# Optimization experiments

Hardware: AMD Instinct MI355X
Metric: run time of the kernel (lower is better)

The kernel has to match this reference:

```python
import jax, jax.numpy as jnp
import numpy as np
import math

S, B, H, NH, HD = 2048, 1, 4096, 32, 128
ROT = HD // 2  # 2D RoPE: each half of head_dim gets its own rotary embedding


def _rotate_half(x):
    x1, x2 = jnp.split(x, 2, axis=-1)
    return jnp.concatenate((-x2, x1), axis=-1)


def _rope_tables(max_pos, dim):
    inv_freq = 1.0 / (10000.0 ** (jnp.arange(0, dim, 2, dtype=jnp.float32) / dim))
    freqs = jnp.arange(max_pos, dtype=jnp.float32)[:, None] * inv_freq[None, :]  # [P, dim/2]
    emb = jnp.concatenate((freqs, freqs), axis=-1)  # [P, dim]
    return jnp.cos(emb), jnp.sin(emb)


def _apply_rope(q, k, cos_t, sin_t, pid):
    # q,k: [S,B,NH,ROT]; pid: [S,B]
    c = cos_t[pid][:, :, None, :]  # [S,B,1,ROT]
    s = sin_t[pid][:, :, None, :]
    return q * c + _rotate_half(q) * s, k * c + _rotate_half(k) * s


def setup_inputs() -> dict:
    key = jax.random.key(0)
    k1, k2, k3, k4, k5 = jax.random.split(key, 5)
    hidden_states = jax.random.normal(k1, (S, B, H), dtype=jnp.float32)
    pos = jnp.arange(S, dtype=jnp.int32)[None, :]          # [1,S] standard positions
    blk = jnp.zeros((1, S), dtype=jnp.int32)                # block positions (pre-gmask all zeros)
    position_ids = jnp.stack([pos, blk], axis=1)            # [B,2,S]
    # causal mask: True = masked out
    attention_mask = jnp.triu(jnp.ones((S, S), dtype=bool), k=1)[None, None]  # [B,1,S,S]
    Wqkv = jax.random.normal(k2, (3 * H, H), dtype=jnp.float32) * 0.02
    bqkv = jax.random.normal(k3, (3 * H,), dtype=jnp.float32) * 0.02
    Wd = jax.random.normal(k4, (H, H), dtype=jnp.float32) * 0.02
    bd = jax.random.normal(k5, (H,), dtype=jnp.float32) * 0.02
    return {"hidden_states": hidden_states, "position_ids": position_ids,
            "attention_mask": attention_mask, "layer_id": 5,
            "Wqkv": Wqkv, "bqkv": bqkv, "Wd": Wd, "bd": bd}


def reference(hidden_states, position_ids, attention_mask, layer_id, Wqkv, bqkv, Wd, bd):
    # QKV projection: [S,B,H] -> [S,B,NH,3*HD]
    mixed = hidden_states @ Wqkv.T + bqkv
    mixed = mixed.reshape(S, B, NH, 3 * HD)
    q, k, v = jnp.split(mixed, 3, axis=-1)  # each [S,B,NH,HD]

    # 2D rotary position embedding on the two head-dim halves
    q1, q2 = jnp.split(q, 2, axis=-1)
    k1, k2 = jnp.split(k, 2, axis=-1)
    cos_t, sin_t = _rope_tables(S, ROT)
    pid = position_ids[:, 0, :].T   # [S,B]
    bid = position_ids[:, 1, :].T   # [S,B]
    q1, k1 = _apply_rope(q1, k1, cos_t, sin_t, pid)
    q2, k2 = _apply_rope(q2, k2, cos_t, sin_t, bid)
    q = jnp.concatenate([q1, q2], axis=-1)
    k = jnp.concatenate([k1, k2], axis=-1)

    # layer-scaled attention scores
    coeff = float(layer_id + 1)
    q = q / (math.sqrt(HD) * coeff)
    scores = jnp.einsum('sbnd,tbnd->bnst', q, k)  # [B,NH,S,S]
    scores = jnp.where(attention_mask, jnp.float32(-10000.0), scores)
    scores = scores.astype(jnp.float32) * coeff
    probs = jax.nn.softmax(scores, axis=-1).astype(hidden_states.dtype)

    ctx = jnp.einsum('bnst,tbnd->sbnd', probs, v).reshape(S, B, NH * HD)
    return ctx @ Wd.T + bd  # [S,B,H]
```

## Files before the change

### kernel.cpp

```cpp
#include <hip/hip_runtime.h>


#define S_LEN 2048
#define NHEAD 32
#define HDIM 128
#define HID 4096

typedef float f32x4 __attribute__((ext_vector_type(4)));
typedef __bf16 bf16x8 __attribute__((ext_vector_type(8)));
typedef __bf16 bf16x4 __attribute__((ext_vector_type(4)));
typedef _Float16 f16x4 __attribute__((ext_vector_type(4)));
typedef _Float16 f16x8 __attribute__((ext_vector_type(8)));

__device__ __forceinline__ void gload16(const void* g, void* l) {
  __builtin_amdgcn_global_load_lds(
      (const __attribute__((address_space(1))) void*)g,
      (__attribute__((address_space(3))) void*)l, 16, 0, 0);
}

__global__ __launch_bounds__(256) void cvt_f32_bf16_kernel(
    const float* __restrict__ in, __bf16* __restrict__ out, int n4) {
  int i = blockIdx.x * 256 + threadIdx.x;
  if (i >= n4) return;
  f32x4 v = *(const f32x4*)(in + (size_t)i * 4);
  bf16x4 o;
  o[0] = (__bf16)v[0]; o[1] = (__bf16)v[1];
  o[2] = (__bf16)v[2]; o[3] = (__bf16)v[3];
  *(bf16x4*)(out + (size_t)i * 4) = o;
}

__device__ __forceinline__ void stage_half(const __bf16* __restrict__ G,
                                           int grow0, int Kstride, int kofs,
                                           __bf16* lds_half, int tid) {
#pragma unroll
  for (int i = 0; i < 2; ++i) {
    int idx = i * 512 + tid;
    int rr = idx >> 3;
    int offp = (idx & 7) * 16;
    int off = offp ^ ((rr & 7) << 4);
    const char* src =
        (const char*)(G + (size_t)(grow0 + rr) * Kstride + kofs) + off;
    char* dst = (char*)lds_half + idx * 16;
    gload16(src, dst);
  }
}

__device__ __forceinline__ bf16x8 ldsfrag(const __bf16* hb, int rowin, int ks,
                                          int lg) {
  int off = ((ks * 64 + lg * 16) ^ ((rowin & 7) << 4));
  return *(const bf16x8*)((const char*)hb + rowin * 128 + off);
}

#define READ_A(DST, SLOT)                                                     \
  _Pragma("unroll") for (int mi = 0; mi < 4; ++mi)                            \
      _Pragma("unroll") for (int ks = 0; ks < 2; ++ks) DST[mi][ks] =          \
      ldsfrag(SLOT, wm * 64 + mi * 16 + lr, ks, lg);

#define READ_B(DST, SLOT)                                                     \
  _Pragma("unroll") for (int nj = 0; nj < 2; ++nj)                            \
      _Pragma("unroll") for (int ks = 0; ks < 2; ++ks) DST[nj][ks] =          \
      ldsfrag(SLOT, wn * 32 + nj * 16 + lr, ks, lg);

#define MFMA_Q(MH, NH, AFR, BFR)                                              \
  __builtin_amdgcn_s_setprio(1);                                              \
  _Pragma("unroll") for (int mi = 0; mi < 4; ++mi)                            \
      _Pragma("unroll") for (int nj = 0; nj < 2; ++nj)                        \
          _Pragma("unroll") for (int ks = 0; ks < 2; ++ks)                    \
              acc[MH][NH][mi][nj] =                                           \
      __builtin_amdgcn_mfma_f32_16x16x32_bf16(AFR[mi][ks], BFR[nj][ks],       \
                                              acc[MH][NH][mi][nj], 0, 0, 0);  \
  __builtin_amdgcn_s_setprio(0);

#define BAR asm volatile("s_barrier" ::: "memory");
#define LGKM0                                                                 \
  asm volatile("s_waitcnt lgkmcnt(0)" ::: "memory");                          \
  __builtin_amdgcn_sched_barrier(0);

template <int OUT_MODE>
__global__ __launch_bounds__(512, 2) void gemm256_kernel(
    const __bf16* __restrict__ A, const __bf16* __restrict__ B,
    const float* __restrict__ bias, void* __restrict__ Cout, int M, int N,
    int Kstride, int klen, int mtiles, int ksplit) {
  __shared__ __align__(16) __bf16 As[2][2][128 * 64];
  __shared__ __align__(16) __bf16 Bs[2][2][128 * 64];
  const int tid = threadIdx.x;
  int bid = blockIdx.x;
  int kh = 0;
  if (ksplit == 2) { kh = bid & 1; bid >>= 1; }
  const int kbase = kh * klen;
  int per_patch = mtiles * 8;
  int p = bid / per_patch, r = bid % per_patch;
  int mt = r % mtiles, nt = p * 8 + r / mtiles;
  int m0 = mt * 256, n0 = nt * 256;
  const int wid = tid >> 6, l = tid & 63;
  const int wm = wid >> 2, wn = wid & 3;
  const int lr = l & 15, lg = l >> 4;
  const int nk = klen >> 6;

  f32x4 acc[2][2][4][2];
#pragma unroll
  for (int a = 0; a < 2; ++a)
#pragma unroll
    for (int b = 0; b < 2; ++b)
#pragma unroll
      for (int c = 0; c < 4; ++c)
#pragma unroll
        for (int d = 0; d < 2; ++d) acc[a][b][c][d] = 0.f;

  stage_half(A, m0, Kstride, kbase, &As[0][0][0], tid);
  stage_half(B, n0, Kstride, kbase, &Bs[0][0][0], tid);
  stage_half(B, n0 + 128, Kstride, kbase, &Bs[0][1][0], tid);
  stage_half(A, m0 + 128, Kstride, kbase, &As[0][1][0], tid);
  if (nk > 1) {
    stage_half(A, m0, Kstride, kbase + 64, &As[1][0][0], tid);
    stage_half(B, n0, Kstride, kbase + 64, &Bs[1][0][0], tid);
    stage_half(B, n0 + 128, Kstride, kbase + 64, &Bs[1][1][0], tid);
    asm volatile("s_waitcnt vmcnt(6)" ::: "memory");
  } else {
    asm volatile("s_waitcnt vmcnt(0)" ::: "memory");
  }
  BAR;

  for (int t = 0; t < nk; ++t) {
    const int cur = t & 1, nxt = cur ^ 1;
    const int kt1 = kbase + (t + 1) * 64;
    const int kt2 = kbase + (t + 2) * 64;
    const bool s1 = (t + 1 < nk), s2 = (t + 2 < nk);
    bf16x8 a[4][2], b0[2][2], b1[2][2];

    READ_A(a, &As[cur][0][0]);
    READ_B(b0, &Bs[cur][0][0]);
    if (s1) stage_half(A, m0 + 128, Kstride, kt1, &As[nxt][1][0], tid);
    BAR;
    LGKM0;
    MFMA_Q(0, 0, a, b0);
    BAR;

    READ_B(b1, &Bs[cur][1][0]);
    if (s2) stage_half(A, m0, Kstride, kt2, &As[cur][0][0], tid);
    BAR;
    LGKM0;
    MFMA_Q(0, 1, a, b1);
    BAR;

    READ_A(a, &As[cur][1][0]);
    if (s2) stage_half(B, n0 + 128, Kstride, kt2, &Bs[cur][1][0], tid);
    BAR;
    LGKM0;
    MFMA_Q(1, 1, a, b1);
    BAR;

    if (s2) stage_half(B, n0, Kstride, kt2, &Bs[cur][0][0], tid);
    BAR;
    MFMA_Q(1, 0, a, b0);
    if (s2)
      asm volatile("s_waitcnt vmcnt(6)" ::: "memory");
    else
      asm volatile("s_waitcnt vmcnt(0)" ::: "memory");
    BAR;
  }

  float* outF = (float*)Cout;
  if (OUT_MODE == 2) outF += (size_t)kh * M * N;
#pragma unroll
  for (int mh = 0; mh < 2; ++mh)
#pragma unroll
    for (int nh = 0; nh < 2; ++nh)
#pragma unroll
      for (int mi = 0; mi < 4; ++mi)
#pragma unroll
        for (int nj = 0; nj < 2; ++nj) {
          int row = m0 + mh * 128 + wm * 64 + mi * 16 + lg * 4;
          int col = n0 + nh * 128 + wn * 32 + nj * 16 + lr;
          float bv = (OUT_MODE == 2) ? 0.f : bias[col];
          f32x4 v = acc[mh][nh][mi][nj];
#pragma unroll
          for (int j = 0; j < 4; ++j) {
            float o = v[j] + bv;
            if (OUT_MODE == 1)
              ((__bf16*)Cout)[(size_t)(row + j) * N + col] = (__bf16)o;
            else
              outF[(size_t)(row + j) * N + col] = o;
          }
        }
}

__global__ __launch_bounds__(256) void reduce_addbias_kernel(
    const float* __restrict__ p0, const float* __restrict__ p1,
    const float* __restrict__ bias, float* __restrict__ out) {
  int i = blockIdx.x * 256 + threadIdx.x;
  int col = (i * 4) & (HID - 1);
  f32x4 a = *(const f32x4*)(p0 + (size_t)i * 4);
  f32x4 b = *(const f32x4*)(p1 + (size_t)i * 4);
  f32x4 c = *(const f32x4*)(bias + col);
  a = a + b + c;
  *(f32x4*)(out + (size_t)i * 4) = a;
}

__global__ __launch_bounds__(256) void rope_kernel(
    const __bf16* __restrict__ qkv, const int* __restrict__ pos_ids,
    __bf16* __restrict__ Q, __bf16* __restrict__ K, _Float16* __restrict__ VT) {
  int h = blockIdx.x & 31, sb = blockIdx.x >> 5;
  int s0 = sb * 64;
  int t = threadIdx.x;
  __shared__ float cs[64][2][2][32];
  __shared__ _Float16 vs[64][132];

  for (int idx = t; idx < 64 * 64; idx += 256) {
    int sl = idx >> 6, half = (idx >> 5) & 1, i = idx & 31;
    int p = pos_ids[half * S_LEN + s0 + sl];
    float f = powf(10000.f, -(float)i / 32.f);
    float ang = (float)p * f;
    cs[sl][half][0][i] = cosf(ang);
    cs[sl][half][1][i] = sinf(ang);
  }
#pragma unroll
  for (int c = 0; c < 4; c++) {
    int chunk = c * 256 + t;
    int slv = chunk >> 4, co = (chunk & 15) * 8;
    const __bf16* vsrc =
        qkv + (size_t)(s0 + slv) * (NHEAD * 3 * HDIM) + h * 384 + 256 + co;
    bf16x8 vv = *(const bf16x8*)vsrc;
    f16x4 a, b;
#pragma unroll
    for (int j = 0; j < 4; j++) {
      a[j] = (_Float16)(float)vv[j];
      b[j] = (_Float16)(float)vv[4 + j];
    }
    *(f16x4*)&vs[slv][co] = a;
    *(f16x4*)&vs[slv][co + 4] = b;
  }
  __syncthreads();

  {
    int sl = t >> 2, role = t & 3;
    int isK = role >> 1, half = role & 1;
    const __bf16* src = qkv + (size_t)(s0 + sl) * (NHEAD * 3 * HDIM) + h * 384 +
                        isK * 128 + half * 64;
    float scale = isK ? 1.f : 0.08838834764831845f;
    float x[64];
    bf16x8 buf[8];
#pragma unroll
    for (int c = 0; c < 8; c++) buf[c] = *(const bf16x8*)(src + c * 8);
#pragma unroll
    for (int c = 0; c < 8; c++)
#pragma unroll
      for (int j = 0; j < 8; j++) x[c * 8 + j] = (float)buf[c][j];
    bf16x8 ob[8];
#pragma unroll
    for (int i = 0; i < 64; i++) {
      int ii = i & 31;
      float cv = cs[sl][half][0][ii], sv = cs[sl][half][1][ii];
      float partner = (i < 32) ? x[i + 32] : x[i - 32];
      float sgn = (i < 32) ? -1.f : 1.f;
      float o = (x[i] * cv + sgn * partner * sv) * scale;
      ob[i >> 3][i & 7] = (__bf16)o;
    }
    __bf16* dst = (isK ? K : Q) + ((size_t)h * S_LEN + s0 + sl) * HDIM + half * 64;
#pragma unroll
    for (int c = 0; c < 8; c++) *(bf16x8*)(dst + c * 8) = ob[c];
  }

#pragma unroll
  for (int c = 0; c < 4; c++) {
    int chunk = c * 256 + t;
    int d = chunk >> 3, so = (chunk & 7) * 8;
    f16x8 o;
#pragma unroll
    for (int j = 0; j < 8; j++) o[j] = vs[so + j][d];
    *(f16x8*)(VT + ((size_t)h * HDIM + d) * S_LEN + s0 + so) = o;
  }
}

__global__ __launch_bounds__(256, 2) void attn_kernel(
    const __bf16* __restrict__ Q, const __bf16* __restrict__ K,
    const _Float16* __restrict__ VT, __bf16* __restrict__ ctx) {
  int b = blockIdx.x;
  int h = b & 31;
  int qb = 15 - (b >> 5);
  int w = threadIdx.x >> 6, l = threadIdx.x & 63;
  int lr = l & 15, lg = l >> 4;
  int q0 = qb * 128 + w * 32;
  const __bf16* Qh = Q + (size_t)h * S_LEN * HDIM;
  const __bf16* Kh = K + (size_t)h * S_LEN * HDIM;
  const _Float16* Vh = VT + (size_t)h * HDIM * S_LEN;

  bf16x8 qfA[4], qfB[4];
#pragma unroll
  for (int kk = 0; kk < 4; kk++) {
    qfA[kk] = *(const bf16x8*)(Qh + (size_t)(q0 + lr) * HDIM + kk * 32 + lg * 8);
    qfB[kk] =
        *(const bf16x8*)(Qh + (size_t)(q0 + 16 + lr) * HDIM + kk * 32 + lg * 8);
  }

  f32x4 accA[8], accB[8];
#pragma unroll
  for (int tt = 0; tt < 8; tt++) { accA[tt] = 0.f; accB[tt] = 0.f; }
  float mA = -INFINITY, lsA = 0.f, mB = -INFINITY, lsB = 0.f;
  int qgA = q0 + lr, qgB = q0 + 16 + lr;
  int qmax = q0 + 31;

  for (int kv0 = 0; kv0 <= qmax; kv0 += 16) {
    f32x4 stA = 0.f, stB = 0.f;
#pragma unroll
    for (int kk = 0; kk < 4; kk++) {
      bf16x8 kf =
          *(const bf16x8*)(Kh + (size_t)(kv0 + lr) * HDIM + kk * 32 + lg * 8);
      stA = __builtin_amdgcn_mfma_f32_16x16x32_bf16(kf, qfA[kk], stA, 0, 0, 0);
      stB = __builtin_amdgcn_mfma_f32_16x16x32_bf16(kf, qfB[kk], stB, 0, 0, 0);
    }
    float tmA = -INFINITY, tmB = -INFINITY;
#pragma unroll
    for (int j = 0; j < 4; j++) {
      int kvg = kv0 + lg * 4 + j;
      if (kvg > qgA) stA[j] = -INFINITY;
      if (kvg > qgB) stB[j] = -INFINITY;
      tmA = fmaxf(tmA, stA[j]);
      tmB = fmaxf(tmB, stB[j]);
    }
    tmA = fmaxf(tmA, __shfl_xor(tmA, 16));
    tmA = fmaxf(tmA, __shfl_xor(tmA, 32));
    tmB = fmaxf(tmB, __shfl_xor(tmB, 16));
    tmB = fmaxf(tmB, __shfl_xor(tmB, 32));
    int need = __any((tmA > mA) || (tmB > mB));
    float mnA = fmaxf(mA, tmA), mnB = fmaxf(mB, tmB);

    f16x4 paA, paB;
    float tsA = 0.f, tsB = 0.f;
#pragma unroll
    for (int j = 0; j < 4; j++) {
      float pA = __expf(stA[j] - mnA);
      float pB = __expf(stB[j] - mnB);
      tsA += pA; tsB += pB;
      paA[j] = (_Float16)pA; paB[j] = (_Float16)pB;
    }
    tsA += __shfl_xor(tsA, 16);
    tsA += __shfl_xor(tsA, 32);
    tsB += __shfl_xor(tsB, 16);
    tsB += __shfl_xor(tsB, 32);

    if (need) {
      float scA = __expf(mA - mnA), scB = __expf(mB - mnB);
      lsA = lsA * scA + tsA;
      lsB = lsB * scB + tsB;
      float sAj[4], sBj[4];
#pragma unroll
      for (int j = 0; j < 4; j++) {
        sAj[j] = __shfl(scA, lg * 4 + j);
        sBj[j] = __shfl(scB, lg * 4 + j);
      }
#pragma unroll
      for (int tt = 0; tt < 8; tt++)
#pragma unroll
        for (int j = 0; j < 4; j++) {
          accA[tt][j] *= sAj[j];
          accB[tt][j] *= sBj[j];
        }
    } else {
      lsA += tsA;
      lsB += tsB;
    }
    mA = mnA; mB = mnB;

#pragma unroll
    for (int tt = 0; tt < 8; tt++) {
      f16x4 vb =
          *(const f16x4*)(Vh + (size_t)(tt * 16 + lr) * S_LEN + kv0 + lg * 4);
      accA[tt] = __builtin_amdgcn_mfma_f32_16x16x16f16(paA, vb, accA[tt], 0, 0, 0);
      accB[tt] = __builtin_amdgcn_mfma_f32_16x16x16f16(paB, vb, accB[tt], 0, 0, 0);
    }
  }

  float rA[4], rB[4];
#pragma unroll
  for (int j = 0; j < 4; j++) {
    rA[j] = 1.f / __shfl(lsA, lg * 4 + j);
    rB[j] = 1.f / __shfl(lsB, lg * 4 + j);
  }
#pragma unroll
  for (int tt = 0; tt < 8; tt++) {
#pragma unroll
    for (int j = 0; j < 4; j++) {
      int qoA = q0 + lg * 4 + j;
      int qoB = q0 + 16 + lg * 4 + j;
      ctx[(size_t)qoA * (NHEAD * HDIM) + h * HDIM + tt * 16 + lr] =
          (__bf16)(accA[tt][j] * rA[j]);
      ctx[(size_t)qoB * (NHEAD * HDIM) + h * HDIM + tt * 16 + lr] =
          (__bf16)(accB[tt][j] * rB[j]);
    }
  }
}

extern "C" void kernel_launch(void* const* d_in, const int* in_sizes, int n_in,
                              void* d_out, int out_size, void* d_ws,
                              size_t ws_size, hipStream_t stream) {
  const float* hs = (const float*)d_in[0];
  const int* pos_ids = (const int*)d_in[1];
  const float* Wqkv = (const float*)d_in[4];
  const float* bqkv = (const float*)d_in[5];
  const float* Wd = (const float*)d_in[6];
  const float* bd = (const float*)d_in[7];
  float* out = (float*)d_out;

  char* ws = (char*)d_ws;
  constexpr size_t OFF_W = 16777216ULL;
  constexpr size_t OFF_QKV = OFF_W + 100663296ULL;
  constexpr size_t OFF_Q = OFF_QKV + 50331648ULL;
  constexpr size_t OFF_K = OFF_Q + 16777216ULL;
  constexpr size_t OFF_V = OFF_K + 16777216ULL;
  __bf16* hsb = (__bf16*)(ws);
  __bf16* wqkvb = (__bf16*)(ws + OFF_W);
  __bf16* wdb = (__bf16*)(ws + OFF_W);
  float* pk = (float*)(ws + OFF_W + 33554432ULL);
  __bf16* qkvb = (__bf16*)(ws + OFF_QKV);
  __bf16* ctxb = qkvb;
  __bf16* Qb = (__bf16*)(ws + OFF_Q);
  __bf16* Kb = (__bf16*)(ws + OFF_K);
  _Float16* Vtb = (_Float16*)(ws + OFF_V);

  cvt_f32_bf16_kernel<<<(S_LEN * HID) / 4 / 256, 256, 0, stream>>>(
      hs, hsb, S_LEN * HID / 4);
  cvt_f32_bf16_kernel<<<(3 * HID * HID) / 4 / 256, 256, 0, stream>>>(
      Wqkv, wqkvb, 3 * HID * HID / 4);

  gemm256_kernel<1><<<8 * 48, 512, 0, stream>>>(hsb, wqkvb, bqkv, qkvb, S_LEN,
                                                3 * HID, HID, HID, 8, 1);

  cvt_f32_bf16_kernel<<<(HID * HID) / 4 / 256, 256, 0, stream>>>(
      Wd, wdb, HID * HID / 4);

  rope_kernel<<<NHEAD * (S_LEN / 64), 256, 0, stream>>>(qkvb, pos_ids, Qb, Kb,
                                                        Vtb);

  attn_kernel<<<NHEAD * (S_LEN / 128), 256, 0, stream>>>(Qb, Kb, Vtb, ctxb);

  gemm256_kernel<2><<<2 * 8 * 16, 512, 0, stream>>>(ctxb, wdb, bd, pk, S_LEN,
                                                    HID, HID, HID / 2, 8, 2);
  reduce_addbias_kernel<<<(S_LEN * HID) / 4 / 256, 256, 0, stream>>>(
      pk, pk + (size_t)S_LEN * HID, bd, out);
}
```

Baseline: 663.7 us.

## Process 32 keys per attention iteration and balance causal block order

The attention inner loop now handles two 16-key tiles per iteration. K and V fragments for both tiles are loaded up front, so more memory requests are in flight and the softmax max/sum reductions and rescale are amortised over twice as many keys. The block-to-query-tile mapping also changes: the second half of the grid goes in ascending order instead of all blocks descending, to spread causal work across waves. The wider step raises register pressure with occupancy 2 per CU, and S_LEN and q tile boundaries are multiples of 32, so masking stays correct.

```diff
diff --git a/kernel.cpp b/kernel.cpp
--- a/kernel.cpp
+++ b/kernel.cpp
@@ -277,7 +277,8 @@
     const _Float16* __restrict__ VT, __bf16* __restrict__ ctx) {
   int b = blockIdx.x;
   int h = b & 31;
-  int qb = 15 - (b >> 5);
+  int x = b >> 5;
+  int qb = (b < 256) ? (15 - x) : (x - 8);
   int w = threadIdx.x >> 6, l = threadIdx.x & 63;
   int lr = l & 15, lg = l >> 4;
   int q0 = qb * 128 + w * 32;
@@ -300,23 +301,39 @@
   int qgA = q0 + lr, qgB = q0 + 16 + lr;
   int qmax = q0 + 31;
 
-  for (int kv0 = 0; kv0 <= qmax; kv0 += 16) {
-    f32x4 stA = 0.f, stB = 0.f;
+  for (int kv0 = 0; kv0 <= qmax; kv0 += 32) {
+    f32x4 stA0 = 0.f, stA1 = 0.f, stB0 = 0.f, stB1 = 0.f;
 #pragma unroll
     for (int kk = 0; kk < 4; kk++) {
-      bf16x8 kf =
+      bf16x8 kf0 =
           *(const bf16x8*)(Kh + (size_t)(kv0 + lr) * HDIM + kk * 32 + lg * 8);
-      stA = __builtin_amdgcn_mfma_f32_16x16x32_bf16(kf, qfA[kk], stA, 0, 0, 0);
-      stB = __builtin_amdgcn_mfma_f32_16x16x32_bf16(kf, qfB[kk], stB, 0, 0, 0);
-    }
+      bf16x8 kf1 = *(const bf16x8*)(Kh + (size_t)(kv0 + 16 + lr) * HDIM +
+                                    kk * 32 + lg * 8);
+      stA0 = __builtin_amdgcn_mfma_f32_16x16x32_bf16(kf0, qfA[kk], stA0, 0, 0, 0);
+      stB0 = __builtin_amdgcn_mfma_f32_16x16x32_bf16(kf0, qfB[kk], stB0, 0, 0, 0);
+      stA1 = __builtin_amdgcn_mfma_f32_16x16x32_bf16(kf1, qfA[kk], stA1, 0, 0, 0);
+      stB1 = __builtin_amdgcn_mfma_f32_16x16x32_bf16(kf1, qfB[kk], stB1, 0, 0, 0);
+    }
+
+    f16x4 vb0[8], vb1[8];
+#pragma unroll
+    for (int tt = 0; tt < 8; tt++) {
+      const _Float16* vcol = Vh + (size_t)(tt * 16 + lr) * S_LEN;
+      vb0[tt] = *(const f16x4*)(vcol + kv0 + lg * 4);
+      vb1[tt] = *(const f16x4*)(vcol + kv0 + 16 + lg * 4);
+    }
+
     float tmA = -INFINITY, tmB = -INFINITY;
 #pragma unroll
     for (int j = 0; j < 4; j++) {
-      int kvg = kv0 + lg * 4 + j;
-      if (kvg > qgA) stA[j] = -INFINITY;
-      if (kvg > qgB) stB[j] = -INFINITY;
-      tmA = fmaxf(tmA, stA[j]);
-      tmB = fmaxf(tmB, stB[j]);
+      int kvg0 = kv0 + lg * 4 + j;
+      int kvg1 = kvg0 + 16;
+      if (kvg0 > qgA) stA0[j] = -INFINITY;
+      if (kvg1 > qgA) stA1[j] = -INFINITY;
+      if (kvg0 > qgB) stB0[j] = -INFINITY;
+      if (kvg1 > qgB) stB1[j] = -INFINITY;
+      tmA = fmaxf(tmA, fmaxf(stA0[j], stA1[j]));
+      tmB = fmaxf(tmB, fmaxf(stB0[j], stB1[j]));
     }
     tmA = fmaxf(tmA, __shfl_xor(tmA, 16));
     tmA = fmaxf(tmA, __shfl_xor(tmA, 32));
@@ -325,14 +342,18 @@
     int need = __any((tmA > mA) || (tmB > mB));
     float mnA = fmaxf(mA, tmA), mnB = fmaxf(mB, tmB);
 
-    f16x4 paA, paB;
+    f16x4 paA0, paA1, paB0, paB1;
     float tsA = 0.f, tsB = 0.f;
 #pragma unroll
     for (int j = 0; j < 4; j++) {
-      float pA = __expf(stA[j] - mnA);
-      float pB = __expf(stB[j] - mnB);
-      tsA += pA; tsB += pB;
-      paA[j] = (_Float16)pA; paB[j] = (_Float16)pB;
+      float pA0 = __expf(stA0[j] - mnA);
+      float pA1 = __expf(stA1[j] - mnA);
+      float pB0 = __expf(stB0[j] - mnB);
+      float pB1 = __expf(stB1[j] - mnB);
+      tsA += pA0 + pA1;
+      tsB += pB0 + pB1;
+      paA0[j] = (_Float16)pA0; paA1[j] = (_Float16)pA1;
+      paB0[j] = (_Float16)pB0; paB1[j] = (_Float16)pB1;
     }
     tsA += __shfl_xor(tsA, 16);
     tsA += __shfl_xor(tsA, 32);
@@ -364,10 +385,14 @@
 
 #pragma unroll
     for (int tt = 0; tt < 8; tt++) {
-      f16x4 vb =
-          *(const f16x4*)(Vh + (size_t)(tt * 16 + lr) * S_LEN + kv0 + lg * 4);
-      accA[tt] = __builtin_amdgcn_mfma_f32_16x16x16f16(paA, vb, accA[tt], 0, 0, 0);
-      accB[tt] = __builtin_amdgcn_mfma_f32_16x16x16f16(paB, vb, accB[tt], 0, 0, 0);
+      accA[tt] =
+          __builtin_amdgcn_mfma_f32_16x16x16f16(paA0, vb0[tt], accA[tt], 0, 0, 0);
+      accB[tt] =
+          __builtin_amdgcn_mfma_f32_16x16x16f16(paB0, vb0[tt], accB[tt], 0, 0, 0);
+      accA[tt] =
+          __builtin_amdgcn_mfma_f32_16x16x16f16(paA1, vb1[tt], accA[tt], 0, 0, 0);
+      accB[tt] =
+          __builtin_amdgcn_mfma_f32_16x16x16f16(paB1, vb1[tt], accB[tt], 0, 0, 0);
     }
   }
 
```

Result: faster. 590.8 us (-11.0%).
